# Performance work log

Measured on AMD Instinct MI355X. Metric: run time of the kernel, lower is better.

## Reference

```python
import jax, jax.numpy as jnp
import numpy as np

D_MODEL = 1024
NUM_HEADS = 16
HEAD_DIM = D_MODEL // NUM_HEADS
CAUSAL = True


def rope_cos_sin(seq_len, dim):
    inv_freq = 1.0 / (10000.0 ** (jnp.arange(0, dim, 2, dtype=jnp.float32) / dim))
    t = jnp.arange(seq_len, dtype=jnp.float32)
    freqs = jnp.einsum('i,j->ij', t, inv_freq)          # [S, dim/2]
    emb = jnp.concatenate([freqs, freqs], axis=-1)      # [S, dim]
    return jnp.cos(emb), jnp.sin(emb)


def rotate_half(x):
    x1, x2 = jnp.split(x, 2, axis=-1)
    return jnp.concatenate([-x2, x1], axis=-1)


def setup_inputs() -> dict:
    key = jax.random.key(0)
    k1, k2, k3, k4, k5 = jax.random.split(key, 5)
    B, S = 2, 2048
    x = jax.random.normal(k1, (B, S, D_MODEL), dtype=jnp.float32)
    s = 1.0 / np.sqrt(D_MODEL)
    W_qkv = jax.random.normal(k2, (D_MODEL, 3 * D_MODEL), dtype=jnp.float32) * s
    b_qkv = jax.random.normal(k3, (3 * D_MODEL,), dtype=jnp.float32) * 0.01
    W_out = jax.random.normal(k4, (D_MODEL, D_MODEL), dtype=jnp.float32) * s
    b_out = jax.random.normal(k5, (D_MODEL,), dtype=jnp.float32) * 0.01
    return {"x": x, "W_qkv": W_qkv, "b_qkv": b_qkv, "W_out": W_out, "b_out": b_out}


def reference(x, W_qkv, b_qkv, W_out, b_out):
    B, S, _ = x.shape
    qkv = x @ W_qkv + b_qkv                              # [B, S, 3D]
    q, k, v = jnp.split(qkv, 3, axis=-1)
    # [B, H, S, hd]
    q = q.reshape(B, S, NUM_HEADS, HEAD_DIM).transpose(0, 2, 1, 3)
    k = k.reshape(B, S, NUM_HEADS, HEAD_DIM).transpose(0, 2, 1, 3)
    v = v.reshape(B, S, NUM_HEADS, HEAD_DIM).transpose(0, 2, 1, 3)
    cos, sin = rope_cos_sin(S, HEAD_DIM)                 # [S, hd]
    cos = cos[None, None]
    sin = sin[None, None]
    q = q * cos + rotate_half(q) * sin
    k = k * cos + rotate_half(k) * sin
    scores = jnp.einsum('bhqd,bhkd->bhqk', q, k) / np.sqrt(HEAD_DIM)
    if CAUSAL:
        causal_mask = jnp.triu(jnp.ones((S, S), dtype=bool), k=1)
        scores = jnp.where(causal_mask, -jnp.inf, scores)
    attn = jax.nn.softmax(scores, axis=-1)
    out = jnp.einsum('bhqk,bhkd->bhqd', attn, v)         # [B, H, S, hd]
    out = out.transpose(0, 2, 1, 3).reshape(B, S, D_MODEL)
    return out @ W_out + b_out
```

## Files before the change

### kernel.cpp

```cpp
#include <hip/hip_runtime.h>
#include <hip/hip_bf16.h>
#include <math.h>

typedef __bf16 bf16;
typedef __bf16 bf16x8 __attribute__((ext_vector_type(8)));
typedef unsigned short ushort8 __attribute__((ext_vector_type(8)));
typedef float floatx4 __attribute__((ext_vector_type(4)));

#define MFMA_BF16(a, b, c) __builtin_amdgcn_mfma_f32_16x16x32_bf16(a, b, c, 0, 0, 0)

#define Q_SCALE 0.18033688011112042f
#define NEG_INVFREQ_LOG2 0.41524101186092029f
#define INV_2PI 0.15915494309189535f

#if __has_builtin(__builtin_amdgcn_exp2f)
#define EXP2F(x) __builtin_amdgcn_exp2f(x)
#else
#define EXP2F(x) exp2f(x)
#endif

__device__ __forceinline__ void hw_sincos_rev(float rev, float* sn, float* cs) {
#if __has_builtin(__builtin_amdgcn_sinf) && __has_builtin(__builtin_amdgcn_cosf) && \
    __has_builtin(__builtin_amdgcn_fractf)
  const float f = __builtin_amdgcn_fractf(rev);
  *sn = __builtin_amdgcn_sinf(f);
  *cs = __builtin_amdgcn_cosf(f);
#else
  sincosf(rev * 6.2831853071795864f, sn, cs);
#endif
}

__device__ __forceinline__ bf16x8 cvt8(const float4 a, const float4 b) {
  bf16x8 t;
  t[0] = (bf16)a.x; t[1] = (bf16)a.y; t[2] = (bf16)a.z; t[3] = (bf16)a.w;
  t[4] = (bf16)b.x; t[5] = (bf16)b.y; t[6] = (bf16)b.z; t[7] = (bf16)b.w;
  return t;
}

__device__ __forceinline__ unsigned int pack2(float a, float b) {
#if __has_builtin(__builtin_amdgcn_cvt_pk_bf16_f32)
  return __builtin_bit_cast(unsigned int, __builtin_amdgcn_cvt_pk_bf16_f32(a, b));
#else
  unsigned short lo = __builtin_bit_cast(unsigned short, (bf16)a);
  unsigned short hi = __builtin_bit_cast(unsigned short, (bf16)b);
  return (unsigned int)lo | ((unsigned int)hi << 16);
#endif
}

__device__ __forceinline__ void gld16(const bf16* g, bf16* l) {
  __builtin_amdgcn_global_load_lds(
      (const __attribute__((address_space(1))) unsigned int*)g,
      (__attribute__((address_space(3))) unsigned int*)l, 16, 0, 0);
}

__device__ __forceinline__ int swz_stage_col(int lane) {
  return ((lane & 3) ^ (((lane >> 2) + (lane >> 4)) & 3)) * 8;
}
__device__ __forceinline__ int swz_read_col(int quad, int c) {
  return (quad ^ ((c + (c >> 2)) & 3)) * 8;
}

__device__ __forceinline__ int xcd_swz(int lin, int n) {
  return (lin & 7) * (n >> 3) + (lin >> 3);
}

__device__ __forceinline__ void transpose_tile(const float* __restrict__ in,
                                               bf16* __restrict__ out, int N,
                                               int K, int n0, int k0, int t,
                                               bf16 (*T)[40]) {
  {
    const int k = t >> 3, n8 = (t & 7) * 8;
    const float* p = &in[(size_t)(k0 + k) * N + n0 + n8];
    const float4 a = *(const float4*)p;
    const float4 b = *(const float4*)(p + 4);
    const float v[8] = {a.x, a.y, a.z, a.w, b.x, b.y, b.z, b.w};
#pragma unroll
    for (int j = 0; j < 8; j++) {
      const int n = n8 + j;
      T[n][k ^ (8 * ((n >> 3) & 3))] = (bf16)v[j];
    }
  }
  __syncthreads();
  {
    const int n = t >> 2, k8 = (t & 3) * 8;
    const int kp = k8 ^ (8 * ((n >> 3) & 3));
    *(bf16x8*)&out[(size_t)(n0 + n) * K + k0 + k8] = *(const bf16x8*)&T[n][kp];
  }
}

__global__ __launch_bounds__(256) void prep_kernel(
    const float* __restrict__ x, bf16* __restrict__ xb,
    const float* __restrict__ Wqkv, bf16* __restrict__ Wqkvt,
    const float* __restrict__ Wout, bf16* __restrict__ Wot) {
  __shared__ __align__(16) bf16 T[64][40];
  const int b = blockIdx.x, t = threadIdx.x;
  if (b < 2048) {
    const int i = b * 256 + t;
    const float4 a = *(const float4*)&x[(size_t)i * 8];
    const float4 d = *(const float4*)&x[(size_t)i * 8 + 4];
    *(bf16x8*)&xb[(size_t)i * 8] = cvt8(a, d);
  } else if (b < 3584) {
    const int idx = b - 2048;
    transpose_tile(Wqkv, Wqkvt, 3072, 1024, (idx % 48) * 64, (idx / 48) * 32, t,
                   T);
  } else {
    const int idx = b - 3584;
    transpose_tile(Wout, Wot, 1024, 1024, (idx % 16) * 64, (idx / 16) * 32, t,
                   T);
  }
}

template <int TN, int MODE>
__global__ __launch_bounds__(256) void gemm_kernel(
    const bf16* __restrict__ A, const bf16* __restrict__ Bt,
    const float* __restrict__ bias, void* __restrict__ out0,
    bf16* __restrict__ outK, bf16* __restrict__ outV, int M, int N, int K) {
  constexpr int NI = TN / 32;
  constexpr int BI = TN / 32;
  __shared__ __align__(16) bf16 As2[2][128][32];
  __shared__ __align__(16) bf16 Bs2[2][TN][32];

  const int tid = threadIdx.x, lane = tid & 63, w = tid >> 6;
  const int c = lane & 15, quad = lane >> 4;
  const int wm = w >> 1, wn = w & 1;
  const int m0 = blockIdx.y * 128, n0 = blockIdx.x * TN;
  const int srow = lane >> 2, scol = swz_stage_col(lane);
  const int rcol = swz_read_col(quad, c);

  floatx4 acc[4][NI] = {};

  for (int k0 = 0; k0 < K; k0 += 64) {
    __syncthreads();
#pragma unroll
    for (int i = 0; i < 4; i++) {
      const int seg = w * 4 + i;
      const int kh = seg >> 3, r0 = (seg & 7) * 16;
      gld16(&A[(size_t)(m0 + r0 + srow) * K + k0 + kh * 32 + scol],
            &As2[kh][r0][0]);
    }
#pragma unroll
    for (int i = 0; i < BI; i++) {
      const int seg = w * BI + i;
      const int kh = seg / (TN / 16), r0 = (seg % (TN / 16)) * 16;
      gld16(&Bt[(size_t)(n0 + r0 + srow) * K + k0 + kh * 32 + scol],
            &Bs2[kh][r0][0]);
    }
    __syncthreads();

#pragma unroll
    for (int kh = 0; kh < 2; kh++) {
      bf16x8 af[4], bfr[NI];
#pragma unroll
      for (int mi = 0; mi < 4; mi++)
        af[mi] = *(const bf16x8*)&As2[kh][wm * 64 + mi * 16 + c][rcol];
#pragma unroll
      for (int ni = 0; ni < NI; ni++)
        bfr[ni] = *(const bf16x8*)&Bs2[kh][wn * (TN / 2) + ni * 16 + c][rcol];
#pragma unroll
      for (int mi = 0; mi < 4; mi++)
#pragma unroll
        for (int ni = 0; ni < NI; ni++)
          acc[mi][ni] = MFMA_BF16(af[mi], bfr[ni], acc[mi][ni]);
    }
  }

  if (MODE == 0) {
#pragma unroll
    for (int mi = 0; mi < 4; mi++)
#pragma unroll
      for (int ni = 0; ni < NI; ni++)
#pragma unroll
        for (int r = 0; r < 4; r++) {
          const int row = m0 + wm * 64 + mi * 16 + quad * 4 + r;
          const int col = n0 + wn * (TN / 2) + ni * 16 + c;
          ((float*)out0)[(size_t)row * N + col] = acc[mi][ni][r] + bias[col];
        }
  } else {
    const int colb = n0 + wn * (TN / 2);
    const int t = colb >> 10;
    const int h = (colb & 1023) >> 6;
    bf16* dst = (t == 0) ? (bf16*)out0 : (t == 1 ? outK : outV);
    if (t == 2) {
#pragma unroll
      for (int ni = 0; ni < NI; ni++) {
        const int d = ni * 16 + c;
        const float bv = bias[colb + ni * 16 + c];
#pragma unroll
        for (int mi = 0; mi < 4; mi++) {
          const int row = m0 + wm * 64 + mi * 16 + quad * 4;
          const int b = row >> 11, s = row & 2047;
          const uint2 u = {pack2(acc[mi][ni][0] + bv, acc[mi][ni][1] + bv),
                           pack2(acc[mi][ni][2] + bv, acc[mi][ni][3] + bv)};
          *(uint2*)&dst[(((size_t)b * 16 + h) * 64 + d) * 2048 + s] = u;
        }
      }
    } else {
      const float qs = (t == 0) ? Q_SCALE : 1.0f;
      const float invr[2] = {exp2f(-NEG_INVFREQ_LOG2 * (float)c) * INV_2PI,
                             exp2f(-NEG_INVFREQ_LOG2 * (float)(16 + c)) * INV_2PI};
#pragma unroll
      for (int mi = 0; mi < 4; mi++) {
#pragma unroll
        for (int r = 0; r < 4; r++) {
          const int row = m0 + wm * 64 + mi * 16 + quad * 4 + r;
          const int b = row >> 11, s = row & 2047;
          const size_t base = (((size_t)b * 16 + h) * 2048 + s) * 64;
#pragma unroll
          for (int ni = 0; ni < 2; ni++) {
            float sn, cs;
            hw_sincos_rev((float)s * invr[ni], &sn, &cs);
            const float v1 = acc[mi][ni][r] + bias[colb + ni * 16 + c];
            const float v2 = acc[mi][ni + 2][r] + bias[colb + (ni + 2) * 16 + c];
            const int d = ni * 16 + c;
            dst[base + d] = (bf16)((v1 * cs - v2 * sn) * qs);
            dst[base + d + 32] = (bf16)((v2 * cs + v1 * sn) * qs);
          }
        }
      }
    }
  }
}

struct AttnState {
  floatx4 o[4];
  floatx4 l;
};

__device__ __forceinline__ void attn_step(
    const bf16x8 qf[2], const bf16x8 kf[4][2], const bf16x8 vf[4][2],
    const bf16x8 ones, bf16 (*PsW)[72], AttnState& st, int qglob, int kbase,
    bool diag, int c, int quad) {
  floatx4 sacc[4] = {};
#pragma unroll
  for (int kg = 0; kg < 4; kg++)
#pragma unroll
    for (int dh = 0; dh < 2; dh++)
      sacc[kg] = MFMA_BF16(kf[kg][dh], qf[dh], sacc[kg]);

#pragma unroll
  for (int kg = 0; kg < 4; kg++) {
    float p[4];
#pragma unroll
    for (int r = 0; r < 4; r++) {
      float e = EXP2F(sacc[kg][r]);
      if (diag && (kbase + kg * 16 + quad * 4 + r > qglob)) e = 0.0f;
      p[r] = e;
    }
    const uint2 u = {pack2(p[0], p[1]), pack2(p[2], p[3])};
    *(uint2*)&PsW[c][kg * 16 + quad * 4] = u;
  }

  bf16x8 pf[2];
#pragma unroll
  for (int ks = 0; ks < 2; ks++)
    pf[ks] = *(const bf16x8*)&PsW[c][ks * 32 + quad * 8];

#pragma unroll
  for (int dg = 0; dg < 4; dg++)
#pragma unroll
    for (int ks = 0; ks < 2; ks++)
      st.o[dg] = MFMA_BF16(vf[dg][ks], pf[ks], st.o[dg]);
  st.l = MFMA_BF16(ones, pf[0], st.l);
  st.l = MFMA_BF16(ones, pf[1], st.l);
}

__global__ __launch_bounds__(512) void attn_kernel(const bf16* __restrict__ Q,
                                                   const bf16* __restrict__ K,
                                                   const bf16* __restrict__ V,
                                                   bf16* __restrict__ Aout) {
  const int S = 2048;
  int p, bh;
  {
    const int n = gridDim.x * gridDim.y;
    const int swz = xcd_swz(blockIdx.x + gridDim.x * blockIdx.y, n);
    p = swz % gridDim.x;
    bh = swz / gridDim.x;
  }
  const int tid = threadIdx.x, lane = tid & 63, wave = tid >> 6;
  const int c = lane & 15, quad = lane >> 4;
  const int grp = wave >> 2, w4 = wave & 3;

  __shared__ __align__(16) bf16 Ks2[2][2][64][32];
  __shared__ __align__(16) bf16 Vt[2][64][64];
  __shared__ __align__(16) bf16 Ps[8][16][72];

  const bf16* Qb = Q + (size_t)bh * S * 64;
  const bf16* Kb = K + (size_t)bh * S * 64;
  const bf16* Vb = V + (size_t)bh * S * 64;
  const int b = bh >> 4, h = bh & 15;

  const int qA = p, qB = 31 - p;
  const int qtile = (grp == 0) ? qB : qA;
  const int qg = qtile * 64 + w4 * 16 + c;

  bf16x8 qf[2];
#pragma unroll
  for (int dh = 0; dh < 2; dh++)
    qf[dh] = *(const bf16x8*)&Qb[(size_t)qg * 64 + dh * 32 + quad * 8];

  bf16x8 ones;
#pragma unroll
  for (int j = 0; j < 8; j++) ones[j] = (bf16)1.0f;

  AttnState st = {};

  const int ksr = lane >> 2, ksc = swz_stage_col(lane);
  const int krcol = swz_read_col(quad, c);
  const int vd = lane >> 3;
  const int vg = lane & 7;

  auto stage = [&](int bb, int kt) {
    const int kt64 = kt * 64;
    {
      const int seg = wave;
      const int dh = seg >> 2, r0 = (seg & 3) * 16;
      gld16(&Kb[(size_t)(kt64 + r0 + ksr) * 64 + dh * 32 + ksc],
            &Ks2[bb][dh][r0][0]);
    }
    {
      const int d0 = wave * 8;
      const int dd = d0 + vd;
      const int g = vg ^ (dd & 7);
      gld16(&Vb[(size_t)dd * 2048 + kt64 + g * 8], &Vt[bb][d0][0]);
    }
  };

  auto load_kf = [&](int bb, bf16x8 (*kf)[2]) {
#pragma unroll
    for (int kg = 0; kg < 4; kg++)
#pragma unroll
      for (int dh = 0; dh < 2; dh++)
        kf[kg][dh] = *(const bf16x8*)&Ks2[bb][dh][kg * 16 + c][krcol];
  };
  auto load_vf = [&](int bb, bf16x8 (*vf)[2]) {
#pragma unroll
    for (int dg = 0; dg < 4; dg++) {
      const int d = dg * 16 + c;
#pragma unroll
      for (int ks = 0; ks < 2; ks++) {
        const int g = (ks * 4 + quad) ^ (c & 7);
        vf[dg][ks] = *(const bf16x8*)&Vt[bb][d][g * 8];
      }
    }
  };

  stage(0, 0);
  __syncthreads();

  int buf = 0;
  for (int kt = 0; kt <= qB; kt++) {
    if (kt < qB) stage(buf ^ 1, kt + 1);
    if (grp == 0 || kt <= qA) {
      bf16x8 kf[4][2], vf[4][2];
      load_kf(buf, kf);
      load_vf(buf, vf);
      attn_step(qf, kf, vf, ones, Ps[wave], st, qg, kt * 64, kt == qtile, c,
                quad);
    }
    __syncthreads();
    buf ^= 1;
  }

  const float iv = 1.0f / st.l[0];
#pragma unroll
  for (int dg = 0; dg < 4; dg++) {
    const uint2 u = {pack2(st.o[dg][0] * iv, st.o[dg][1] * iv),
                     pack2(st.o[dg][2] * iv, st.o[dg][3] * iv)};
    *(uint2*)&Aout[((size_t)b * 2048 + qg) * 1024 + h * 64 + dg * 16 + quad * 4] = u;
  }
}

extern "C" void kernel_launch(void* const* d_in, const int* in_sizes, int n_in,
                              void* d_out, int out_size, void* d_ws,
                              size_t ws_size, hipStream_t stream) {
  const float* x = (const float*)d_in[0];
  const float* W_qkv = (const float*)d_in[1];
  const float* b_qkv = (const float*)d_in[2];
  const float* W_out = (const float*)d_in[3];
  const float* b_out = (const float*)d_in[4];
  float* out = (float*)d_out;

  const int B = 2, S = 2048, NH = 16;
  const size_t qn = (size_t)B * NH * S * 64;

  bf16* xb = (bf16*)d_ws;
  bf16* Wqkvt = xb + qn;
  bf16* Wot = Wqkvt + 3072 * 1024;
  bf16* Qw = Wot + 1024 * 1024;
  bf16* Kw = Qw + qn;
  bf16* Vw = Kw + qn;
  bf16* AO = xb;

  prep_kernel<<<dim3(4096), 256, 0, stream>>>(x, xb, W_qkv, Wqkvt, W_out, Wot);

  gemm_kernel<128, 1><<<dim3(3072 / 128, 4096 / 128), 256, 0, stream>>>(
      xb, Wqkvt, b_qkv, Qw, Kw, Vw, 4096, 3072, 1024);
  attn_kernel<<<dim3(16, B * NH), 512, 0, stream>>>(Qw, Kw, Vw, AO);
  gemm_kernel<64, 0><<<dim3(1024 / 64, 4096 / 128), 256, 0, stream>>>(
      AO, Wot, b_out, out, nullptr, nullptr, 4096, 1024, 1024);
}
```

Measured before the change: 189.7 us.

## Split attention into one q-tile per block, swizzle P smem, deepen out-proj K tile

The attention kernel previously paired two query tiles (p and 31-p) inside a 512-thread block to balance causal work. It now launches one 256-thread block per query tile, ordered so heavy and light tiles interleave. This removes idle waves in the light group but doubles K/V staging per query tile. The P scratch buffer drops its padding and uses an XOR swizzle to avoid LDS bank conflicts. The output-projection GEMM now stages K in chunks of 128 instead of 64, halving its barrier count.

```diff
diff --git a/kernel.cpp b/kernel.cpp
--- a/kernel.cpp
+++ b/kernel.cpp
@@ -110,15 +110,16 @@
   }
 }
 
-template <int TN, int MODE>
+template <int TN, int MODE, int BK>
 __global__ __launch_bounds__(256) void gemm_kernel(
     const bf16* __restrict__ A, const bf16* __restrict__ Bt,
     const float* __restrict__ bias, void* __restrict__ out0,
     bf16* __restrict__ outK, bf16* __restrict__ outV, int M, int N, int K) {
   constexpr int NI = TN / 32;
-  constexpr int BI = TN / 32;
-  __shared__ __align__(16) bf16 As2[2][128][32];
-  __shared__ __align__(16) bf16 Bs2[2][TN][32];
+  constexpr int AL = BK / 16;
+  constexpr int BL = (TN * BK) / 2048;
+  __shared__ __align__(16) bf16 As2[BK / 32][128][32];
+  __shared__ __align__(16) bf16 Bs2[BK / 32][TN][32];
 
   const int tid = threadIdx.x, lane = tid & 63, w = tid >> 6;
   const int c = lane & 15, quad = lane >> 4;
@@ -129,18 +130,18 @@
 
   floatx4 acc[4][NI] = {};
 
-  for (int k0 = 0; k0 < K; k0 += 64) {
+  for (int k0 = 0; k0 < K; k0 += BK) {
     __syncthreads();
 #pragma unroll
-    for (int i = 0; i < 4; i++) {
-      const int seg = w * 4 + i;
+    for (int i = 0; i < AL; i++) {
+      const int seg = w * AL + i;
       const int kh = seg >> 3, r0 = (seg & 7) * 16;
       gld16(&A[(size_t)(m0 + r0 + srow) * K + k0 + kh * 32 + scol],
             &As2[kh][r0][0]);
     }
 #pragma unroll
-    for (int i = 0; i < BI; i++) {
-      const int seg = w * BI + i;
+    for (int i = 0; i < BL; i++) {
+      const int seg = w * BL + i;
       const int kh = seg / (TN / 16), r0 = (seg % (TN / 16)) * 16;
       gld16(&Bt[(size_t)(n0 + r0 + srow) * K + k0 + kh * 32 + scol],
             &Bs2[kh][r0][0]);
@@ -148,7 +149,7 @@
     __syncthreads();
 
 #pragma unroll
-    for (int kh = 0; kh < 2; kh++) {
+    for (int kh = 0; kh < BK / 32; kh++) {
       bf16x8 af[4], bfr[NI];
 #pragma unroll
       for (int mi = 0; mi < 4; mi++)
@@ -228,8 +229,9 @@
 
 __device__ __forceinline__ void attn_step(
     const bf16x8 qf[2], const bf16x8 kf[4][2], const bf16x8 vf[4][2],
-    const bf16x8 ones, bf16 (*PsW)[72], AttnState& st, int qglob, int kbase,
+    const bf16x8 ones, bf16 (*PsW)[64], AttnState& st, int qglob, int kbase,
     bool diag, int c, int quad) {
+  const int cx = (c & 7) << 3;
   floatx4 sacc[4] = {};
 #pragma unroll
   for (int kg = 0; kg < 4; kg++)
@@ -247,13 +249,13 @@
       p[r] = e;
     }
     const uint2 u = {pack2(p[0], p[1]), pack2(p[2], p[3])};
-    *(uint2*)&PsW[c][kg * 16 + quad * 4] = u;
+    *(uint2*)&PsW[c][(kg * 16 + quad * 4) ^ cx] = u;
   }
 
   bf16x8 pf[2];
 #pragma unroll
   for (int ks = 0; ks < 2; ks++)
-    pf[ks] = *(const bf16x8*)&PsW[c][ks * 32 + quad * 8];
+    pf[ks] = *(const bf16x8*)&PsW[c][(ks * 32 + quad * 8) ^ cx];
 
 #pragma unroll
   for (int dg = 0; dg < 4; dg++)
@@ -264,34 +266,32 @@
   st.l = MFMA_BF16(ones, pf[1], st.l);
 }
 
-__global__ __launch_bounds__(512) void attn_kernel(const bf16* __restrict__ Q,
+__global__ __launch_bounds__(256) void attn_kernel(const bf16* __restrict__ Q,
                                                    const bf16* __restrict__ K,
                                                    const bf16* __restrict__ V,
                                                    bf16* __restrict__ Aout) {
   const int S = 2048;
-  int p, bh;
+  int qt, bh;
   {
-    const int n = gridDim.x * gridDim.y;
-    const int swz = xcd_swz(blockIdx.x + gridDim.x * blockIdx.y, n);
-    p = swz % gridDim.x;
-    bh = swz / gridDim.x;
+    const int lin = blockIdx.x + gridDim.x * blockIdx.y;
+    const int swz = xcd_swz(lin, 1024);
+    bh = swz >> 5;
+    const int r5 = swz & 31;
+    qt = (r5 & 1) ? (r5 >> 1) : 31 - (r5 >> 1);
   }
   const int tid = threadIdx.x, lane = tid & 63, wave = tid >> 6;
   const int c = lane & 15, quad = lane >> 4;
-  const int grp = wave >> 2, w4 = wave & 3;
 
   __shared__ __align__(16) bf16 Ks2[2][2][64][32];
   __shared__ __align__(16) bf16 Vt[2][64][64];
-  __shared__ __align__(16) bf16 Ps[8][16][72];
+  __shared__ __align__(16) bf16 Ps[4][16][64];
 
   const bf16* Qb = Q + (size_t)bh * S * 64;
   const bf16* Kb = K + (size_t)bh * S * 64;
   const bf16* Vb = V + (size_t)bh * S * 64;
   const int b = bh >> 4, h = bh & 15;
 
-  const int qA = p, qB = 31 - p;
-  const int qtile = (grp == 0) ? qB : qA;
-  const int qg = qtile * 64 + w4 * 16 + c;
+  const int qg = qt * 64 + wave * 16 + c;
 
   bf16x8 qf[2];
 #pragma unroll
@@ -311,14 +311,16 @@
 
   auto stage = [&](int bb, int kt) {
     const int kt64 = kt * 64;
-    {
-      const int seg = wave;
+#pragma unroll
+    for (int i = 0; i < 2; i++) {
+      const int seg = wave * 2 + i;
       const int dh = seg >> 2, r0 = (seg & 3) * 16;
       gld16(&Kb[(size_t)(kt64 + r0 + ksr) * 64 + dh * 32 + ksc],
             &Ks2[bb][dh][r0][0]);
     }
-    {
-      const int d0 = wave * 8;
+#pragma unroll
+    for (int i = 0; i < 2; i++) {
+      const int d0 = wave * 16 + i * 8;
       const int dd = d0 + vd;
       const int g = vg ^ (dd & 7);
       gld16(&Vb[(size_t)dd * 2048 + kt64 + g * 8], &Vt[bb][d0][0]);
@@ -348,15 +350,12 @@
   __syncthreads();
 
   int buf = 0;
-  for (int kt = 0; kt <= qB; kt++) {
-    if (kt < qB) stage(buf ^ 1, kt + 1);
-    if (grp == 0 || kt <= qA) {
-      bf16x8 kf[4][2], vf[4][2];
-      load_kf(buf, kf);
-      load_vf(buf, vf);
-      attn_step(qf, kf, vf, ones, Ps[wave], st, qg, kt * 64, kt == qtile, c,
-                quad);
-    }
+  for (int kt = 0; kt <= qt; kt++) {
+    if (kt < qt) stage(buf ^ 1, kt + 1);
+    bf16x8 kf[4][2], vf[4][2];
+    load_kf(buf, kf);
+    load_vf(buf, vf);
+    attn_step(qf, kf, vf, ones, Ps[wave], st, qg, kt * 64, kt == qt, c, quad);
     __syncthreads();
     buf ^= 1;
   }
@@ -393,9 +392,9 @@
 
   prep_kernel<<<dim3(4096), 256, 0, stream>>>(x, xb, W_qkv, Wqkvt, W_out, Wot);
 
-  gemm_kernel<128, 1><<<dim3(3072 / 128, 4096 / 128), 256, 0, stream>>>(
+  gemm_kernel<128, 1, 64><<<dim3(3072 / 128, 4096 / 128), 256, 0, stream>>>(
       xb, Wqkvt, b_qkv, Qw, Kw, Vw, 4096, 3072, 1024);
-  attn_kernel<<<dim3(16, B * NH), 512, 0, stream>>>(Qw, Kw, Vw, AO);
-  gemm_kernel<64, 0><<<dim3(1024 / 64, 4096 / 128), 256, 0, stream>>>(
+  attn_kernel<<<dim3(32, B * NH), 256, 0, stream>>>(Qw, Kw, Vw, AO);
+  gemm_kernel<64, 0, 128><<<dim3(1024 / 64, 4096 / 128), 256, 0, stream>>>(
       AO, Wot, b_out, out, nullptr, nullptr, 4096, 1024, 1024);
 }
```

Result: slower. 201.0 us (+6.0%).
